# Performance work log

Measured on AMD Instinct MI355X. Metric: run time of the kernel, lower is better.

Reference implementation:

```python
import jax, jax.numpy as jnp
import numpy as np

B, H, W, C = 4, 64, 64, 512
CR = C // 8  # reduced channel dim for query/key (conv_b, conv_c)


def setup_inputs() -> dict:
    key = jax.random.key(0)
    k1, k2, k3, k4, k5 = jax.random.split(key, 5)
    x = jax.random.normal(k1, (B, H, W, C), dtype=jnp.float32)
    # 1x1 conv kernels (no bias) == dense weights applied per pixel
    Wb = jax.random.normal(k2, (C, CR), dtype=jnp.float32) * (2.0 / C) ** 0.5
    Wc = jax.random.normal(k3, (C, CR), dtype=jnp.float32) * (2.0 / C) ** 0.5
    Wd = jax.random.normal(k4, (C, C), dtype=jnp.float32) * (2.0 / C) ** 0.5
    gamma = jax.random.normal(k5, (1,), dtype=jnp.float32)
    return {"x": x, "Wb": Wb, "Wc": Wc, "Wd": Wd, "gamma": gamma}


def reference(x, Wb, Wc, Wd, gamma):
    b, h, w, c = x.shape
    n = h * w
    xf = x.reshape(b, n, c)                       # [B,N,C] flatten spatial
    q = jnp.einsum('bnc,cd->bnd', xf, Wb)         # conv_b: [B,N,CR]
    k = jnp.einsum('bnc,cd->bnd', xf, Wc)         # conv_c: [B,N,CR]
    v = jnp.einsum('bnc,cd->bnd', xf, Wd)         # conv_d: [B,N,C]
    scores = jnp.einsum('bnd,bmd->bnm', q, k)     # [B,N,N] position affinities
    attn = jax.nn.softmax(scores, axis=-1)
    out = jnp.einsum('bnm,bmc->bnc', attn, v)     # [B,N,C]
    out = out.reshape(b, h, w, c)
    return gamma * out + x
```

## Files before the change

### kernel.cpp

```cpp
#include <hip/hip_runtime.h>


typedef __bf16 bf16_t;
typedef __bf16 bf16x8 __attribute__((ext_vector_type(8)));
typedef float f32x4 __attribute__((ext_vector_type(4)));
typedef unsigned long long u64;

#define NN 4096
#define CC 512
#define VSTRIDE 4160u
#define PSTRIDE 4160u
#define ESHIFT 90.0f

#define OFF_QH 0u
#define OFF_QL 1048576u
#define OFF_KH 2097152u
#define OFF_KL 3145728u
#define OFF_VT 4194304u
#define OFF_WBH 29491200u
#define OFF_WBL 29523968u
#define OFF_WCH 29556736u
#define OFF_WCL 29589504u
#define OFF_WD  29622272u
#define OFF_P   12713984u
#define PBATCH  17039360u

static __device__ __forceinline__ f32x4 mfma16(bf16x8 a, bf16x8 b, f32x4 c) {
    return __builtin_amdgcn_mfma_f32_16x16x32_bf16(a, b, c, 0, 0, 0);
}

static __device__ __forceinline__ void load_lds16(const bf16_t* g, bf16_t* l) {
    __builtin_amdgcn_global_load_lds(
        (const __attribute__((address_space(1))) unsigned int*)g,
        (__attribute__((address_space(3))) unsigned int*)l, 16, 0, 0);
}

__global__ __launch_bounds__(256) void prep_kernel(const float* __restrict__ Wb,
                                                   const float* __restrict__ Wc,
                                                   const float* __restrict__ Wd,
                                                   bf16_t* __restrict__ ws) {
    int j = blockIdx.x * 256 + threadIdx.x;
    if (j < 32768) {
        int n = j >> 9, k = j & 511;
        float v = Wb[k * 64 + n];
        bf16_t h = (bf16_t)v;
        ws[OFF_WBH + j] = h;
        ws[OFF_WBL + j] = (bf16_t)(v - (float)h);
    } else if (j < 65536) {
        int j2 = j - 32768;
        int n = j2 >> 9, k = j2 & 511;
        float v = Wc[k * 64 + n];
        bf16_t h = (bf16_t)v;
        ws[OFF_WCH + j2] = h;
        ws[OFF_WCL + j2] = (bf16_t)(v - (float)h);
    } else if (j < 327680) {
        int j2 = j - 65536;
        int n = j2 >> 9, k = j2 & 511;
        ws[OFF_WD + j2] = (bf16_t)Wd[k * 512 + n];
    }
}

__global__ __launch_bounds__(256, 1) void qkv_kernel(const float* __restrict__ x,
                                                     bf16_t* __restrict__ ws) {
    int mt = blockIdx.x;
    int tid = threadIdx.x;
    int w = tid >> 6, lane = tid & 63, quad = lane >> 4, l16 = lane & 15;

    __shared__ __align__(16) bf16_t Vs[64][72];

    const float* xrow = x + (size_t)(mt * 64 + w * 16 + l16) * 512 + quad * 8;
    bf16x8 xh[16], xl[16];
#pragma unroll
    for (int ks = 0; ks < 16; ++ks) {
        f32x4 a0 = *(const f32x4*)(xrow + ks * 32);
        f32x4 a1 = *(const f32x4*)(xrow + ks * 32 + 4);
#pragma unroll
        for (int j = 0; j < 4; ++j) {
            bf16_t h0 = (bf16_t)a0[j];
            bf16_t h1 = (bf16_t)a1[j];
            xh[ks][j] = h0;     xl[ks][j] = (bf16_t)(a0[j] - (float)h0);
            xh[ks][4 + j] = h1; xl[ks][4 + j] = (bf16_t)(a1[j] - (float)h1);
        }
    }

    for (int nT = 0; nT < 2; ++nT) {
        const bf16_t* wh = ws + (nT == 0 ? OFF_WBH : OFF_WCH);
        const bf16_t* wl = ws + (nT == 0 ? OFF_WBL : OFF_WCL);
        f32x4 acc[4];
#pragma unroll
        for (int nt = 0; nt < 4; ++nt) acc[nt] = (f32x4){0.f, 0.f, 0.f, 0.f};
#pragma unroll
        for (int ks = 0; ks < 16; ++ks) {
#pragma unroll
            for (int nt = 0; nt < 4; ++nt) {
                size_t wo = (size_t)(nt * 16 + l16) * 512 + ks * 32 + quad * 8;
                bf16x8 bh = *(const bf16x8*)(wh + wo);
                bf16x8 bl = *(const bf16x8*)(wl + wo);
                acc[nt] = mfma16(xh[ks], bh, acc[nt]);
                acc[nt] = mfma16(xh[ks], bl, acc[nt]);
                acc[nt] = mfma16(xl[ks], bh, acc[nt]);
            }
        }
        unsigned base_h = (nT == 0) ? OFF_QH : OFF_KH;
        unsigned base_l = (nT == 0) ? OFF_QL : OFF_KL;
#pragma unroll
        for (int nt = 0; nt < 4; ++nt) {
            int gc = nt * 16 + l16;
#pragma unroll
            for (int r = 0; r < 4; ++r) {
                int gr = mt * 64 + w * 16 + quad * 4 + r;
                int b = gr >> 12, np = gr & 4095;
                float v = acc[nt][r];
                bf16_t h = (bf16_t)v;
                size_t o = ((size_t)(b * 4096 + np)) * 64 + gc;
                ws[base_h + o] = h;
                ws[base_l + o] = (bf16_t)(v - (float)h);
            }
        }
    }

    for (int nT = 0; nT < 8; ++nT) {
        const bf16_t* wp = ws + OFF_WD + (size_t)nT * 64 * 512;
        f32x4 acc[4];
#pragma unroll
        for (int nt = 0; nt < 4; ++nt) acc[nt] = (f32x4){0.f, 0.f, 0.f, 0.f};
#pragma unroll
        for (int ks = 0; ks < 16; ++ks) {
#pragma unroll
            for (int nt = 0; nt < 4; ++nt) {
                bf16x8 bb = *(const bf16x8*)(wp + (size_t)(nt * 16 + l16) * 512 + ks * 32 + quad * 8);
                acc[nt] = mfma16(xh[ks], bb, acc[nt]);
            }
        }
#pragma unroll
        for (int nt = 0; nt < 4; ++nt) {
            bf16_t pk[4];
#pragma unroll
            for (int r = 0; r < 4; ++r) pk[r] = (bf16_t)acc[nt][r];
            *(u64*)&Vs[nt * 16 + l16][w * 16 + quad * 4] = *(u64*)pk;
        }
        __syncthreads();
        int gr0 = mt * 64;
        int bb = gr0 >> 12, np0 = gr0 & 4095;
        int ch = tid >> 2, seg = tid & 3;
        f32x4 d0 = *(const f32x4*)&Vs[ch][seg * 16];
        f32x4 d1 = *(const f32x4*)&Vs[ch][seg * 16 + 8];
        bf16_t* dst = ws + OFF_VT +
            ((size_t)bb * 512 + (size_t)(nT * 64 + ch)) * VSTRIDE + np0 + seg * 16;
        *(f32x4*)(dst) = d0;
        *(f32x4*)(dst + 8) = d1;
        __syncthreads();
    }
}

__global__ __launch_bounds__(256, 2) void score_kernel(bf16_t* __restrict__ ws) {
    int idx = blockIdx.x;
    int mt = idx & 31;
    int nt = (idx >> 5) & 31;
    int b  = idx >> 10;
    int tid = threadIdx.x;
    int w = tid >> 6, lane = tid & 63, quad = lane >> 4, l16 = lane & 15;
    int wr = w >> 1, wc = w & 1;

    __shared__ __align__(16) bf16_t Ls[128][136];

    const bf16_t* Qh = ws + OFF_QH + (size_t)b * NN * 64;
    const bf16_t* Ql = ws + OFF_QL + (size_t)b * NN * 64;
    const bf16_t* Kh = ws + OFF_KH + (size_t)b * NN * 64;
    const bf16_t* Kl = ws + OFF_KL + (size_t)b * NN * 64;

    bf16x8 qh[4][2], ql[4][2];
#pragma unroll
    for (int rt = 0; rt < 4; ++rt) {
        size_t qo = (size_t)(nt * 128 + wr * 64 + rt * 16 + l16) * 64 + quad * 8;
        qh[rt][0] = *(const bf16x8*)(Qh + qo);
        qh[rt][1] = *(const bf16x8*)(Qh + qo + 32);
        ql[rt][0] = *(const bf16x8*)(Ql + qo);
        ql[rt][1] = *(const bf16x8*)(Ql + qo + 32);
    }

    f32x4 s[4][4];
#pragma unroll
    for (int ct = 0; ct < 4; ++ct) {
        size_t ko = (size_t)(mt * 128 + wc * 64 + ct * 16 + l16) * 64 + quad * 8;
        bf16x8 kh0 = *(const bf16x8*)(Kh + ko);
        bf16x8 kh1 = *(const bf16x8*)(Kh + ko + 32);
        bf16x8 kl0 = *(const bf16x8*)(Kl + ko);
        bf16x8 kl1 = *(const bf16x8*)(Kl + ko + 32);
#pragma unroll
        for (int rt = 0; rt < 4; ++rt) {
            f32x4 a = (f32x4){0.f, 0.f, 0.f, 0.f};
            a = mfma16(qh[rt][0], kh0, a);
            a = mfma16(qh[rt][1], kh1, a);
            a = mfma16(qh[rt][0], kl0, a);
            a = mfma16(qh[rt][1], kl1, a);
            a = mfma16(ql[rt][0], kh0, a);
            a = mfma16(ql[rt][1], kh1, a);
            s[rt][ct] = a;
        }
    }

#pragma unroll
    for (int rt = 0; rt < 4; ++rt)
#pragma unroll
        for (int ct = 0; ct < 4; ++ct)
#pragma unroll
            for (int r = 0; r < 4; ++r) {
                float p = __expf(s[rt][ct][r] - ESHIFT);
                Ls[wr * 64 + rt * 16 + quad * 4 + r][wc * 64 + ct * 16 + l16] = (bf16_t)p;
            }
    __syncthreads();

    bf16_t* P = ws + OFF_P + (size_t)b * PBATCH;
    int row0 = tid >> 4, chunk = tid & 15;
#pragma unroll
    for (int it = 0; it < 8; ++it) {
        int row = it * 16 + row0;
        f32x4 d = *(const f32x4*)&Ls[row][chunk * 8];
        *(f32x4*)(P + (size_t)(nt * 128 + row) * PSTRIDE + mt * 128 + chunk * 8) = d;
    }
}

__global__ __launch_bounds__(256, 2) void pv_kernel(const float* __restrict__ x,
                                                    const float* __restrict__ gamma_p,
                                                    const bf16_t* __restrict__ ws,
                                                    float* __restrict__ out) {
    int idx = blockIdx.x;
    int ct4 = idx & 3;
    int b   = (idx >> 2) & 3;
    int nt  = idx >> 4;
    int tid = threadIdx.x;
    int w = tid >> 6, lane = tid & 63, quad = lane >> 4, l16 = lane & 15;
    int wr = w >> 1, wc = w & 1;

    __shared__ __align__(16) bf16_t Pt_s[4096];
    __shared__ __align__(16) bf16_t Vt_s[4096];
    __shared__ __align__(16) float rsum_s[128];

    const bf16_t* P = ws + OFF_P + (size_t)b * PBATCH + (size_t)(nt * 128) * PSTRIDE;
    const bf16_t* V = ws + OFF_VT + (size_t)b * CC * VSTRIDE + (size_t)(ct4 * 128) * VSTRIDE;

    f32x4 o[4][4];
#pragma unroll
    for (int rt = 0; rt < 4; ++rt)
#pragma unroll
        for (int ct = 0; ct < 4; ++ct) o[rt][ct] = (f32x4){0.f, 0.f, 0.f, 0.f};
    f32x4 osum[4];
#pragma unroll
    for (int rt = 0; rt < 4; ++rt) osum[rt] = (f32x4){0.f, 0.f, 0.f, 0.f};

    bf16_t onev = (bf16_t)1.0f;
    bf16x8 vones = {onev, onev, onev, onev, onev, onev, onev, onev};

    int prow = tid >> 2;
    int pch  = tid & 3;
    const bf16_t* gp0 = P + (size_t)prow * PSTRIDE + pch * 8;
    const bf16_t* gp1 = P + (size_t)(prow + 64) * PSTRIDE + pch * 8;
    const bf16_t* gv0 = V + (size_t)prow * VSTRIDE + pch * 8;
    const bf16_t* gv1 = V + (size_t)(prow + 64) * VSTRIDE + pch * 8;

    for (int k = 0; k < 128; ++k) {
        int m0 = k * 32;
        load_lds16(gp0 + m0, &Pt_s[tid * 8]);
        load_lds16(gp1 + m0, &Pt_s[2048 + tid * 8]);
        load_lds16(gv0 + m0, &Vt_s[tid * 8]);
        load_lds16(gv1 + m0, &Vt_s[2048 + tid * 8]);
        __syncthreads();

        bf16x8 pa[4], vb[4];
#pragma unroll
        for (int rt = 0; rt < 4; ++rt)
            pa[rt] = *(const bf16x8*)&Pt_s[(wr * 64 + rt * 16 + l16) * 32 + quad * 8];
#pragma unroll
        for (int ct = 0; ct < 4; ++ct)
            vb[ct] = *(const bf16x8*)&Vt_s[(wc * 64 + ct * 16 + l16) * 32 + quad * 8];
#pragma unroll
        for (int ct = 0; ct < 4; ++ct)
#pragma unroll
            for (int rt = 0; rt < 4; ++rt)
                o[rt][ct] = mfma16(pa[rt], vb[ct], o[rt][ct]);
        if (wc == 0) {
#pragma unroll
            for (int rt = 0; rt < 4; ++rt) osum[rt] = mfma16(pa[rt], vones, osum[rt]);
        }
        __syncthreads();
    }

    if (wc == 0 && l16 == 0) {
#pragma unroll
        for (int rt = 0; rt < 4; ++rt)
#pragma unroll
            for (int r = 0; r < 4; ++r)
                rsum_s[wr * 64 + rt * 16 + quad * 4 + r] = osum[rt][r];
    }
    __syncthreads();

    float g = gamma_p[0];
#pragma unroll
    for (int rt = 0; rt < 4; ++rt) {
        f32x4 rs = *(const f32x4*)&rsum_s[wr * 64 + rt * 16 + quad * 4];
        f32x4 linv;
#pragma unroll
        for (int r = 0; r < 4; ++r) linv[r] = 1.0f / rs[r];
#pragma unroll
        for (int ct = 0; ct < 4; ++ct) {
#pragma unroll
            for (int r = 0; r < 4; ++r) {
                int n = nt * 128 + wr * 64 + rt * 16 + quad * 4 + r;
                int c = ct4 * 128 + wc * 64 + ct * 16 + l16;
                size_t off = ((size_t)(b * 4096 + n)) * 512 + c;
                out[off] = g * (o[rt][ct][r] * linv[r]) + x[off];
            }
        }
    }
}

extern "C" void kernel_launch(void* const* d_in, const int* in_sizes, int n_in,
                              void* d_out, int out_size, void* d_ws, size_t ws_size,
                              hipStream_t stream) {
    const float* x     = (const float*)d_in[0];
    const float* Wb    = (const float*)d_in[1];
    const float* Wc    = (const float*)d_in[2];
    const float* Wd    = (const float*)d_in[3];
    const float* gamma = (const float*)d_in[4];
    bf16_t* ws = (bf16_t*)d_ws;
    float* out = (float*)d_out;

    prep_kernel<<<1280, 256, 0, stream>>>(Wb, Wc, Wd, ws);
    qkv_kernel<<<256, 256, 0, stream>>>(x, ws);
    score_kernel<<<4096, 256, 0, stream>>>(ws);
    pv_kernel<<<512, 256, 0, stream>>>(x, gamma, ws, out);
}
```

Baseline: 358.3 us.

## Double-buffer PV kernel LDS tiles with 64-wide K steps and XOR swizzle

The P·V kernel now stages P and V tiles into two alternating LDS buffers, so the next 64-column chunk loads while MFMAs run on the current one. The K step doubles from 32 to 64, which halves the number of barriers. LDS reads use an XOR swizzle on the chunk index to avoid bank conflicts. The row-sum scratch now aliases the first P buffer. The cost is 64KB of LDS per block, which may limit occupancy.

```diff
diff --git a/kernel.cpp b/kernel.cpp
--- a/kernel.cpp
+++ b/kernel.cpp
@@ -233,13 +233,17 @@
     int w = tid >> 6, lane = tid & 63, quad = lane >> 4, l16 = lane & 15;
     int wr = w >> 1, wc = w & 1;
 
-    __shared__ __align__(16) bf16_t Pt_s[4096];
-    __shared__ __align__(16) bf16_t Vt_s[4096];
-    __shared__ __align__(16) float rsum_s[128];
+    __shared__ __align__(16) bf16_t Pt[2][8192];
+    __shared__ __align__(16) bf16_t Vt[2][8192];
 
     const bf16_t* P = ws + OFF_P + (size_t)b * PBATCH + (size_t)(nt * 128) * PSTRIDE;
     const bf16_t* V = ws + OFF_VT + (size_t)b * CC * VSTRIDE + (size_t)(ct4 * 128) * VSTRIDE;
 
+    int sr = tid >> 3;
+    int sc = (tid & 7) ^ (sr & 7);
+    const bf16_t* gp = P + (size_t)sr * PSTRIDE + sc * 8;
+    const bf16_t* gv = V + (size_t)sr * VSTRIDE + sc * 8;
+
     f32x4 o[4][4];
 #pragma unroll
     for (int rt = 0; rt < 4; ++rt)
@@ -252,40 +256,58 @@
     bf16_t onev = (bf16_t)1.0f;
     bf16x8 vones = {onev, onev, onev, onev, onev, onev, onev, onev};
 
-    int prow = tid >> 2;
-    int pch  = tid & 3;
-    const bf16_t* gp0 = P + (size_t)prow * PSTRIDE + pch * 8;
-    const bf16_t* gp1 = P + (size_t)(prow + 64) * PSTRIDE + pch * 8;
-    const bf16_t* gv0 = V + (size_t)prow * VSTRIDE + pch * 8;
-    const bf16_t* gv1 = V + (size_t)(prow + 64) * VSTRIDE + pch * 8;
-
-    for (int k = 0; k < 128; ++k) {
-        int m0 = k * 32;
-        load_lds16(gp0 + m0, &Pt_s[tid * 8]);
-        load_lds16(gp1 + m0, &Pt_s[2048 + tid * 8]);
-        load_lds16(gv0 + m0, &Vt_s[tid * 8]);
-        load_lds16(gv1 + m0, &Vt_s[2048 + tid * 8]);
+    auto stage = [&](int buf, int t) {
+        int m0 = t * 64;
+        load_lds16(gp + m0,                  &Pt[buf][tid * 8]);
+        load_lds16(gp + 32u * PSTRIDE + m0,  &Pt[buf][2048 + tid * 8]);
+        load_lds16(gp + 64u * PSTRIDE + m0,  &Pt[buf][4096 + tid * 8]);
+        load_lds16(gp + 96u * PSTRIDE + m0,  &Pt[buf][6144 + tid * 8]);
+        load_lds16(gv + m0,                  &Vt[buf][tid * 8]);
+        load_lds16(gv + 32u * VSTRIDE + m0,  &Vt[buf][2048 + tid * 8]);
+        load_lds16(gv + 64u * VSTRIDE + m0,  &Vt[buf][4096 + tid * 8]);
+        load_lds16(gv + 96u * VSTRIDE + m0,  &Vt[buf][6144 + tid * 8]);
+    };
+
+    auto compute = [&](int buf) {
+#pragma unroll
+        for (int kk = 0; kk < 2; ++kk) {
+            bf16x8 pa[4], vb[4];
+#pragma unroll
+            for (int rt = 0; rt < 4; ++rt) {
+                int R = wr * 64 + rt * 16 + l16;
+                int mc = (kk * 4 + quad) ^ (R & 7);
+                pa[rt] = *(const bf16x8*)&Pt[buf][R * 64 + mc * 8];
+            }
+#pragma unroll
+            for (int ct = 0; ct < 4; ++ct) {
+                int Rv = wc * 64 + ct * 16 + l16;
+                int mc = (kk * 4 + quad) ^ (Rv & 7);
+                vb[ct] = *(const bf16x8*)&Vt[buf][Rv * 64 + mc * 8];
+            }
+#pragma unroll
+            for (int ct = 0; ct < 4; ++ct)
+#pragma unroll
+                for (int rt = 0; rt < 4; ++rt)
+                    o[rt][ct] = mfma16(pa[rt], vb[ct], o[rt][ct]);
+            if (wc == 0) {
+#pragma unroll
+                for (int rt = 0; rt < 4; ++rt)
+                    osum[rt] = mfma16(pa[rt], vones, osum[rt]);
+            }
+        }
+    };
+
+    stage(0, 0);
+    __syncthreads();
+    for (int t = 0; t < 63; ++t) {
+        int cur = t & 1;
+        stage(cur ^ 1, t + 1);
+        compute(cur);
         __syncthreads();
-
-        bf16x8 pa[4], vb[4];
-#pragma unroll
-        for (int rt = 0; rt < 4; ++rt)
-            pa[rt] = *(const bf16x8*)&Pt_s[(wr * 64 + rt * 16 + l16) * 32 + quad * 8];
-#pragma unroll
-        for (int ct = 0; ct < 4; ++ct)
-            vb[ct] = *(const bf16x8*)&Vt_s[(wc * 64 + ct * 16 + l16) * 32 + quad * 8];
-#pragma unroll
-        for (int ct = 0; ct < 4; ++ct)
-#pragma unroll
-            for (int rt = 0; rt < 4; ++rt)
-                o[rt][ct] = mfma16(pa[rt], vb[ct], o[rt][ct]);
-        if (wc == 0) {
-#pragma unroll
-            for (int rt = 0; rt < 4; ++rt) osum[rt] = mfma16(pa[rt], vones, osum[rt]);
-        }
-        __syncthreads();
-    }
-
+    }
+    compute(1);
+
+    float* rsum_s = (float*)&Pt[0][0];
     if (wc == 0 && l16 == 0) {
 #pragma unroll
         for (int rt = 0; rt < 4; ++rt)
```

Result: faster. 341.0 us (-4.8%).
